# Optimization experiments

Hardware: AMD Instinct MI355X
Metric: run time of the kernel (lower is better)

The kernel has to match this reference:

```python
import jax, jax.numpy as jnp
import numpy as np
from jax import lax

STRIDES = (8, 8, 16, 32, 32)
GRIDS = (40, 36, 24, 16, 12)
MIN_SCORE = 0.1
KEEP_SCORE = 0.1
MASK_THR = 0.5
UPDATE_THR = 0.05
SIGMA = 2.0
TOPN = 500
MAX_MASKS = 100
UP = 4


def points_nms(h):
    # max_pool2d(k=2, s=1, p=1) then crop last row/col == pad (1,0) window 2
    m = lax.reduce_window(h, -jnp.inf, lax.max, (1, 1, 2, 2), (1, 1, 1, 1),
                          ((0, 0), (0, 0), (1, 0), (1, 0)))
    return h * (m == h).astype(h.dtype)


def resize_mat(insz, outsz):
    # bilinear align_corners=True interpolation matrix [outsz, insz]
    if outsz > 1:
        src = jnp.arange(outsz, dtype=jnp.float32) * ((insz - 1) / (outsz - 1))
    else:
        src = jnp.zeros((outsz,), jnp.float32)
    lo = jnp.clip(jnp.floor(src).astype(jnp.int32), 0, insz - 1)
    hi = jnp.minimum(lo + 1, insz - 1)
    w = src - lo.astype(jnp.float32)
    r = jnp.arange(outsz)
    M = jnp.zeros((outsz, insz), jnp.float32)
    return M.at[r, lo].add(1.0 - w).at[r, hi].add(w)


def bilinear(x, oh, ow):  # x: [k,h,w]
    Mh = resize_mat(x.shape[1], oh)
    Mw = resize_mat(x.shape[2], ow)
    return jnp.einsum('Ww,kHw->kHW', Mw, jnp.einsum('Hh,khw->kHw', Mh, x))


def prep(cate_preds, kernel_preds):
    B = cate_preds[0].shape[0]
    cate = [points_nms(jax.nn.sigmoid(c)) for c in cate_preds]
    cate_flat = jnp.concatenate(
        [jnp.transpose(c, (0, 2, 3, 1)).reshape(B, -1, c.shape[1]) for c in cate], axis=1)
    kern_flat = jnp.concatenate(
        [jnp.transpose(k, (0, 2, 3, 1)).reshape(B, -1, k.shape[1]) for k in kernel_preds], axis=1)
    strides_vec = jnp.concatenate(
        [jnp.full((g * g,), float(s), jnp.float32) for g, s in zip(GRIDS, STRIDES)])
    return cate_flat, kern_flat, strides_vec


def decode_soft(mask_feat, cate_flat, kern_flat, strides_vec):
    # fixed-shape (padded) version of the per-image decode; invalid slots carry score 0
    nc = cate_flat.shape[-1]
    flat = cate_flat.reshape(-1)
    vals, idx = lax.top_k(jnp.where(flat > MIN_SCORE, flat, -1.0), TOPN)
    validk = vals > MIN_SCORE
    cell = idx // nc
    label = idx % nc
    # dynamic 1x1 conv == einsum with gathered kernels
    sig = jax.nn.sigmoid(jnp.einsum('kc,chw->khw', kern_flat[cell], mask_feat))
    binm = (sig > MASK_THR).astype(sig.dtype)
    summ = binm.sum((1, 2))
    keep = validk & (summ > strides_vec[cell])
    seg = (sig * binm).sum((1, 2)) / jnp.maximum(summ, 1e-6)
    scores = jnp.where(keep, vals * seg, 0.0)
    order = jnp.argsort(-scores)
    scores = scores[order]
    sig = sig[order]
    label = label[order]
    keep_o = keep[order]
    summ = jnp.where(keep, summ, 0.0)[order]
    binm = binm[order] * keep_o[:, None, None].astype(binm.dtype)
    # matrix NMS (gaussian)
    flatm = binm.reshape(TOPN, -1)
    inter = flatm @ flatm.T
    iou = inter / jnp.maximum(summ[:, None] + summ[None, :] - inter, 1e-6)
    triu = jnp.triu(jnp.ones((TOPN, TOPN), bool), 1)
    dmat = jnp.where(triu & (label[:, None] == label[None, :]), iou, 0.0)
    comp = dmat.max(0)  # max suppression each item received
    coef = (jnp.exp(-SIGMA * dmat**2) / jnp.exp(-SIGMA * comp[:, None]**2)).min(0)
    s2 = scores * coef
    s2 = jnp.where((s2 >= UPDATE_THR) & (s2 >= KEEP_SCORE) & keep_o, s2, 0.0)
    fv, fi = lax.top_k(s2, MAX_MASKS)
    return fv, jnp.where(fv > 0, label[fi], -1), sig[fi]


def reference(mask_feat_pred, cate_pred_0, cate_pred_1, cate_pred_2, cate_pred_3,
              cate_pred_4, kernel_pred_0, kernel_pred_1, kernel_pred_2, kernel_pred_3,
              kernel_pred_4, scaled_sizes, origin_sizes):
    cate_preds = [cate_pred_0, cate_pred_1, cate_pred_2, cate_pred_3, cate_pred_4]
    kernel_preds = [kernel_pred_0, kernel_pred_1, kernel_pred_2, kernel_pred_3, kernel_pred_4]
    cate_flat, kern_flat, sv = prep(cate_preds, kernel_preds)
    fv, lab, sig = jax.vmap(lambda mf, cf, kf: decode_soft(mf, cf, kf, sv))(
        mask_feat_pred, cate_flat, kern_flat)
    H = mask_feat_pred.shape[2] * UP
    W = mask_feat_pred.shape[3] * UP
    up = jax.vmap(lambda s: bilinear(s, H, W))(sig)  # [B,M,H,W]
    sh, sw = int(scaled_sizes[0, 0]), int(scaled_sizes[0, 1])
    oh, ow = int(origin_sizes[0, 0]), int(origin_sizes[0, 1])
    up = up[:, :, :sh, :sw]
    up = jax.vmap(lambda s: bilinear(s, oh, ow))(up)
    masks = ((up > MASK_THR) & (fv > 0)[:, :, None, None]).astype(jnp.uint8)
    return masks, lab, fv


def setup_inputs() -> dict:
    key = jax.random.key(0)
    ks = jax.random.split(key, 11)
    B, C, NC, HM = 2, 256, 80, 128
    inp = {'mask_feat_pred': jax.random.normal(ks[0], (B, C, HM, HM), jnp.float32)}
    for i, g in enumerate(GRIDS):
        inp[f'cate_pred_{i}'] = jax.random.normal(ks[1 + i], (B, NC, g, g), jnp.float32)
        inp[f'kernel_pred_{i}'] = jax.random.normal(ks[6 + i], (B, C, g, g), jnp.float32) * 0.05
    inp['scaled_sizes'] = jnp.full((B, 2), HM * UP, jnp.int32)
    inp['origin_sizes'] = jnp.full((B, 2), HM * UP, jnp.int32)
    return inp
```

## Files before the change

### kernel.cpp

```cpp
#include <hip/hip_runtime.h>
#include <math.h>
#include <stdint.h>

#define NBATCH 2
#define NC 80
#define CHN 256
#define HMM 128
#define HWN (HMM*HMM)
#define NCELL 3872
#define FLATN (NCELL*NC)
#define TOPN 500
#define SROWS 512
#define MAXM 100
#define OUTH 512
#define OUTW 512
#define NBINS 1024
#define CANDCAP 2048
#define BM 128
#define BN2 256
#define BK 32
#define GNB (HWN/BN2)

__device__ __forceinline__ float sigmoidf_(float x){ return 1.0f/(1.0f+expf(-x)); }

__device__ __forceinline__ void cell_decode(int cell, int& lvl, int& g, int& y, int& x){
  int off;
  if (cell < 1600)      { lvl=0; g=40; off=0; }
  else if (cell < 2896) { lvl=1; g=36; off=1600; }
  else if (cell < 3472) { lvl=2; g=24; off=2896; }
  else if (cell < 3728) { lvl=3; g=16; off=3472; }
  else                  { lvl=4; g=12; off=3728; }
  int r = cell - off; y = r / g; x = r - y*g;
}

template<int N, int NT>
__device__ __forceinline__ void bitonic_desc(uint64_t* key){
  int tid = threadIdx.x;
  for (int k = 2; k <= N; k <<= 1)
    for (int j = k >> 1; j > 0; j >>= 1) {
      __syncthreads();
      for (int e = tid; e < N; e += NT) {
        int l = e ^ j;
        if (l > e) {
          uint64_t a = key[e], c = key[l];
          bool up = ((e & k) == 0);
          if (up ? (a < c) : (a > c)) { key[e] = c; key[l] = a; }
        }
      }
    }
  __syncthreads();
}

__global__ void k0_init(uint32_t* hist, uint32_t* cnt){
  int t = blockIdx.x*blockDim.x + threadIdx.x;
  if (t < NBATCH*NBINS) hist[t] = 0;
  if (t < NBATCH) cnt[t] = 0;
}

__global__ void k1_scores(const float* __restrict__ c0, const float* __restrict__ c1,
                          const float* __restrict__ c2, const float* __restrict__ c3,
                          const float* __restrict__ c4,
                          float* __restrict__ scores, uint32_t* __restrict__ hist){
  int t = blockIdx.x*blockDim.x + threadIdx.x;
  if (t >= NBATCH*FLATN) return;
  int b = t / FLATN;
  int rem = t - b*FLATN;
  int cell = rem / NC;
  int c = rem - cell*NC;
  int lvl,g,y,x; cell_decode(cell,lvl,g,y,x);
  const float* cp = lvl==0?c0:lvl==1?c1:lvl==2?c2:lvl==3?c3:c4;
  const float* base = cp + (size_t)(b*NC + c)*g*g;
  float raw = base[y*g + x];
  float m = raw;
  if (y > 0)          m = fmaxf(m, base[(y-1)*g + x]);
  if (x > 0)          m = fmaxf(m, base[y*g + x-1]);
  if (y > 0 && x > 0) m = fmaxf(m, base[(y-1)*g + x-1]);
  float s = (raw == m) ? sigmoidf_(raw) : 0.0f;
  scores[t] = s;
  if (s > 0.1f) {
    int bin = (int)(s * 1024.0f); if (bin > NBINS-1) bin = NBINS-1;
    atomicAdd(&hist[b*NBINS + bin], 1u);
  }
}

__global__ __launch_bounds__(1024) void k2_cutoff(const uint32_t* __restrict__ hist, int* __restrict__ cutoff){
  __shared__ uint32_t h[NBINS];
  int b = blockIdx.x;
  h[threadIdx.x] = hist[b*NBINS + threadIdx.x];
  __syncthreads();
  if (threadIdx.x == 0) {
    int acc = 0; int cut = 0;
    for (int d = NBINS-1; d >= 0; --d) {
      acc += (int)h[d];
      if (acc >= TOPN) { cut = d; break; }
    }
    cutoff[b] = cut;
  }
}

__global__ void k3_gather(const float* __restrict__ scores, const int* __restrict__ cutoff,
                          uint32_t* __restrict__ cnt, float* __restrict__ cval, uint32_t* __restrict__ cidx){
  int t = blockIdx.x*blockDim.x + threadIdx.x;
  if (t >= NBATCH*FLATN) return;
  int b = t / FLATN; int idx = t - b*FLATN;
  float v = scores[t];
  if (v > 0.1f) {
    int bin = (int)(v * 1024.0f); if (bin > NBINS-1) bin = NBINS-1;
    if (bin >= cutoff[b]) {
      uint32_t p = atomicAdd(&cnt[b], 1u);
      if (p < CANDCAP) { cval[b*CANDCAP+p] = v; cidx[b*CANDCAP+p] = (uint32_t)idx; }
    }
  }
}

__global__ __launch_bounds__(1024) void k4_sort(const uint32_t* __restrict__ cnt,
        const float* __restrict__ cval, const uint32_t* __restrict__ cidx,
        float* __restrict__ vals, int* __restrict__ cellA, int* __restrict__ labelA){
  __shared__ uint64_t key[CANDCAP];
  int b = blockIdx.x; int tid = threadIdx.x;
  int n = (int)cnt[b]; if (n > CANDCAP) n = CANDCAP;
  for (int e = tid; e < CANDCAP; e += 1024) {
    uint64_t k = 0;
    if (e < n)
      k = ((uint64_t)__float_as_uint(cval[b*CANDCAP+e]) << 32) |
          (uint64_t)(0xFFFFFFFFu - cidx[b*CANDCAP+e]);
    key[e] = k;
  }
  bitonic_desc<CANDCAP,1024>(key);
  for (int r = tid; r < TOPN; r += 1024) {
    uint64_t k = key[r];
    if ((k >> 32) == 0) { vals[b*TOPN+r] = -1.0f; cellA[b*TOPN+r] = 0; labelA[b*TOPN+r] = 0; }
    else {
      uint32_t idx = 0xFFFFFFFFu - (uint32_t)(k & 0xFFFFFFFFu);
      vals[b*TOPN+r]   = __uint_as_float((uint32_t)(k >> 32));
      cellA[b*TOPN+r]  = (int)(idx / NC);
      labelA[b*TOPN+r] = (int)(idx % NC);
    }
  }
}

__global__ void k5_kmat(const float* __restrict__ k0p, const float* __restrict__ k1p,
                        const float* __restrict__ k2p, const float* __restrict__ k3p,
                        const float* __restrict__ k4p,
                        const int* __restrict__ cellA, float* __restrict__ Kmat){
  int t = blockIdx.x*blockDim.x + threadIdx.x;
  if (t >= NBATCH*TOPN*CHN) return;
  int b = t / (TOPN*CHN); int rem = t - b*(TOPN*CHN);
  int k = rem / CHN; int c = rem - k*CHN;
  int cell = cellA[b*TOPN + k];
  int lvl,g,y,x; cell_decode(cell,lvl,g,y,x);
  const float* kp = lvl==0?k0p:lvl==1?k1p:lvl==2?k2p:lvl==3?k3p:k4p;
  Kmat[t] = kp[((size_t)(b*CHN + c)*g + y)*g + x];
}

__global__ __launch_bounds__(256, 2) void k6_gemm1(const float* __restrict__ Kmat, const float* __restrict__ mf,
        float* __restrict__ sigfull, uint32_t* __restrict__ bits,
        float* __restrict__ psum, float* __restrict__ pseg){
  __shared__ alignas(16) float As[BK][BM+4];
  __shared__ alignas(16) float Bs[BK][BN2];
  __shared__ uint32_t bitsL[BM][8];
  int tid = threadIdx.x;
  int nb = blockIdx.x, mb = blockIdx.y, b = blockIdx.z;
  int row0 = mb*BM, col0 = nb*BN2;
  int tx = tid & 15, ty = tid >> 4;
  for (int i = tid; i < BM*8; i += 256) ((uint32_t*)bitsL)[i] = 0;

  int ar[4], aq[4], bkk[8], bcc[8];
  #pragma unroll
  for (int i = 0; i < 4; ++i) { int e = i*256 + tid; ar[i] = e >> 3; aq[i] = e & 7; }
  #pragma unroll
  for (int i = 0; i < 8; ++i) { int e = i*256 + tid; bkk[i] = e >> 6; bcc[i] = e & 63; }

  float4 pa[4], pb[8];
  const float4 z4 = make_float4(0.f,0.f,0.f,0.f);
  #pragma unroll
  for (int i = 0; i < 4; ++i) {
    int rr = row0 + ar[i];
    pa[i] = (rr < TOPN) ? *(const float4*)&Kmat[((size_t)b*TOPN + rr)*CHN + aq[i]*4] : z4;
  }
  #pragma unroll
  for (int i = 0; i < 8; ++i)
    pb[i] = *(const float4*)&mf[((size_t)b*CHN + bkk[i])*HWN + col0 + bcc[i]*4];

  float acc[8][16];
  #pragma unroll
  for (int i=0;i<8;i++)
    #pragma unroll
    for(int j=0;j<16;j++) acc[i][j]=0.f;

  for (int k0 = 0; k0 < CHN; k0 += BK) {
    __syncthreads();
    #pragma unroll
    for (int i = 0; i < 4; ++i) {
      int colA = ar[i] ^ (aq[i] << 2);
      As[aq[i]*4+0][colA] = pa[i].x;
      As[aq[i]*4+1][colA] = pa[i].y;
      As[aq[i]*4+2][colA] = pa[i].z;
      As[aq[i]*4+3][colA] = pa[i].w;
    }
    #pragma unroll
    for (int i = 0; i < 8; ++i)
      *(float4*)&Bs[bkk[i]][bcc[i]*4] = pb[i];
    __syncthreads();
    if (k0 + BK < CHN) {
      int k0n = k0 + BK;
      #pragma unroll
      for (int i = 0; i < 4; ++i) {
        int rr = row0 + ar[i];
        pa[i] = (rr < TOPN) ? *(const float4*)&Kmat[((size_t)b*TOPN + rr)*CHN + k0n + aq[i]*4] : z4;
      }
      #pragma unroll
      for (int i = 0; i < 8; ++i)
        pb[i] = *(const float4*)&mf[((size_t)b*CHN + k0n + bkk[i])*HWN + col0 + bcc[i]*4];
    }
    #pragma unroll 2
    for (int kk = 0; kk < BK; ++kk) {
      int s = (kk >> 2) << 2;
      float4 a0 = *(float4*)&As[kk][(ty*8) ^ s];
      float4 a1 = *(float4*)&As[kk][(ty*8+4) ^ s];
      float av[8] = {a0.x,a0.y,a0.z,a0.w,a1.x,a1.y,a1.z,a1.w};
      #pragma unroll
      for (int q = 0; q < 4; ++q) {
        float4 bv = *(float4*)&Bs[kk][q*64 + tx*4];
        #pragma unroll
        for (int i = 0; i < 8; ++i) {
          acc[i][q*4+0] += av[i]*bv.x;
          acc[i][q*4+1] += av[i]*bv.y;
          acc[i][q*4+2] += av[i]*bv.z;
          acc[i][q*4+3] += av[i]*bv.w;
        }
      }
    }
  }
  #pragma unroll
  for (int i = 0; i < 8; ++i) {
    int r = row0 + ty*8 + i;
    float se = 0.f; int cc = 0;
    #pragma unroll
    for (int q = 0; q < 4; ++q) {
      float4 sv;
      sv.x = sigmoidf_(acc[i][q*4+0]);
      sv.y = sigmoidf_(acc[i][q*4+1]);
      sv.z = sigmoidf_(acc[i][q*4+2]);
      sv.w = sigmoidf_(acc[i][q*4+3]);
      uint32_t m = 0;
      if (sv.x > 0.5f) { m |= 1u; se += sv.x; cc++; }
      if (sv.y > 0.5f) { m |= 2u; se += sv.y; cc++; }
      if (sv.z > 0.5f) { m |= 4u; se += sv.z; cc++; }
      if (sv.w > 0.5f) { m |= 8u; se += sv.w; cc++; }
      atomicOr(&bitsL[ty*8+i][2*q + (tx>>3)], m << ((tx&7)*4));
      *(float4*)&sigfull[((size_t)b*SROWS + r)*HWN + col0 + q*64 + tx*4] = sv;
    }
    #pragma unroll
    for (int d = 1; d < 16; d <<= 1) {
      se += __shfl_xor(se, d);
      cc += __shfl_xor(cc, d);
    }
    if (tx == 0 && r < TOPN) {
      psum[((size_t)b*TOPN + r)*GNB + nb] = (float)cc;
      pseg[((size_t)b*TOPN + r)*GNB + nb] = se;
    }
  }
  __syncthreads();
  for (int e = tid; e < BM*8; e += 256) {
    int rr = e >> 3, w = e & 7;
    if (row0 + rr < TOPN)
      bits[((size_t)b*TOPN + row0 + rr)*512 + nb*8 + w] = bitsL[rr][w];
  }
}

__global__ void k7_rowstats(const float* __restrict__ psum, const float* __restrict__ pseg,
                            const float* __restrict__ vals, const int* __restrict__ cellA,
                            float* __restrict__ summ, float* __restrict__ scores, int* __restrict__ keepA){
  int t = blockIdx.x*blockDim.x + threadIdx.x;
  if (t >= NBATCH*TOPN) return;
  float sc = 0.f, sg = 0.f;
  for (int i = 0; i < GNB; i += 4) {
    float4 a = *(const float4*)&psum[(size_t)t*GNB+i];
    float4 c = *(const float4*)&pseg[(size_t)t*GNB+i];
    sc += a.x+a.y+a.z+a.w; sg += c.x+c.y+c.z+c.w;
  }
  float v = vals[t];
  int cell = cellA[t];
  int lvl,g,y,x; cell_decode(cell,lvl,g,y,x);
  float stride = (lvl<=1)?8.f:(lvl==2)?16.f:32.f;
  bool keep = (v > 0.1f) && (sc > stride);
  float seg = sg / fmaxf(sc, 1e-6f);
  summ[t] = sc;
  scores[t] = keep ? v*seg : 0.f;
  keepA[t] = keep ? 1 : 0;
}

__global__ __launch_bounds__(512) void k8_order(const float* __restrict__ scores, int* __restrict__ order){
  __shared__ uint64_t key[512];
  int b = blockIdx.x, tid = threadIdx.x;
  uint64_t k = 0;
  if (tid < TOPN)
    k = ((uint64_t)__float_as_uint(scores[b*TOPN+tid]) << 32) | (uint64_t)(0xFFFFFFFFu - (uint32_t)tid);
  key[tid] = k;
  bitonic_desc<512,512>(key);
  if (tid < TOPN) order[b*TOPN+tid] = (int)(0xFFFFFFFFu - (uint32_t)(key[tid] & 0xFFFFFFFFu));
}

__global__ __launch_bounds__(256) void k9_dmat(const uint32_t* __restrict__ bitsG,
        const int* __restrict__ order, const int* __restrict__ labelA, const int* __restrict__ keepA,
        const float* __restrict__ summ, float* __restrict__ dmatT){
  __shared__ uint32_t rowb[512];
  int i = blockIdx.x, b = blockIdx.y, tid = threadIdx.x;
  int oi = order[b*TOPN + i];
  if (!keepA[b*TOPN + oi]) return;
  float si = summ[b*TOPN + oi];
  int li = labelA[b*TOPN + oi];
  for (int w = tid; w < 512; w += 256) rowb[w] = bitsG[((size_t)b*TOPN + oi)*512 + w];
  __syncthreads();
  for (int j = i + 1 + tid; j < TOPN; j += 256) {
    int oj = order[b*TOPN + j];
    if (!keepA[b*TOPN + oj] || labelA[b*TOPN + oj] != li) continue;
    const uint4* rj = (const uint4*)&bitsG[((size_t)b*TOPN + oj)*512];
    const uint4* ri = (const uint4*)rowb;
    int cc = 0;
    for (int w = 0; w < 128; ++w) {
      uint4 x = rj[w], y = ri[w];
      cc += __popc(x.x & y.x) + __popc(x.y & y.y) + __popc(x.z & y.z) + __popc(x.w & y.w);
    }
    float sj = summ[b*TOPN + oj];
    float inter = (float)cc;
    dmatT[((size_t)b*TOPN + j)*TOPN + i] = inter / fmaxf(si + sj - inter, 1e-6f);
  }
}

__global__ __launch_bounds__(256) void k10_comp(const float* __restrict__ dmatT,
        float* __restrict__ comp, float* __restrict__ e2c){
  __shared__ float red[4];
  int j = blockIdx.x, b = blockIdx.y, tid = threadIdx.x;
  float m = 0.f;
  for (int i = tid; i < TOPN; i += 256) m = fmaxf(m, dmatT[((size_t)b*TOPN+j)*TOPN + i]);
  #pragma unroll
  for (int d = 1; d < 64; d <<= 1) m = fmaxf(m, __shfl_xor(m, d));
  if ((tid & 63) == 0) red[tid >> 6] = m;
  __syncthreads();
  if (tid == 0) {
    m = fmaxf(fmaxf(red[0], red[1]), fmaxf(red[2], red[3]));
    comp[b*TOPN+j] = m;
    e2c[b*TOPN+j] = expf(-2.0f*m*m);
  }
}

__global__ __launch_bounds__(256) void k10_coef(const float* __restrict__ dmatT, const float* __restrict__ e2c,
        const float* __restrict__ scores, const int* __restrict__ order, const int* __restrict__ keepA,
        float* __restrict__ s2){
  __shared__ float red[4];
  int j = blockIdx.x, b = blockIdx.y, tid = threadIdx.x;
  float mn = 1e30f;
  for (int i = tid; i < TOPN; i += 256) {
    float d = dmatT[((size_t)b*TOPN+j)*TOPN + i];
    float r = expf(-2.0f*d*d) / e2c[b*TOPN+i];
    mn = fminf(mn, r);
  }
  #pragma unroll
  for (int d = 1; d < 64; d <<= 1) mn = fminf(mn, __shfl_xor(mn, d));
  if ((tid & 63) == 0) red[tid >> 6] = mn;
  __syncthreads();
  if (tid == 0) {
    mn = fminf(fminf(red[0], red[1]), fminf(red[2], red[3]));
    int oj = order[b*TOPN+j];
    float s = scores[b*TOPN+oj] * mn;
    bool ok = (s >= 0.05f) && (s >= 0.1f) && (keepA[b*TOPN+oj] != 0);
    s2[b*TOPN+j] = ok ? s : 0.f;
  }
}

__global__ __launch_bounds__(512) void k11_top100(const float* __restrict__ s2, const int* __restrict__ order,
        const int* __restrict__ labelA, float* __restrict__ outF, int* __restrict__ selrow){
  __shared__ uint64_t key[512];
  int b = blockIdx.x, tid = threadIdx.x;
  uint64_t k = 0;
  if (tid < TOPN)
    k = ((uint64_t)__float_as_uint(s2[b*TOPN+tid]) << 32) | (uint64_t)(0xFFFFFFFFu - (uint32_t)tid);
  key[tid] = k;
  bitonic_desc<512,512>(key);
  if (tid < MAXM) {
    uint64_t kk = key[tid];
    float v = __uint_as_float((uint32_t)(kk >> 32));
    int j = (int)(0xFFFFFFFFu - (uint32_t)(kk & 0xFFFFFFFFu));
    if (j < 0 || j >= TOPN) { j = 0; v = 0.f; }
    int orow = order[b*TOPN + j];
    float lab = (v > 0.f) ? (float)labelA[b*TOPN + orow] : -1.0f;
    size_t maskCount = (size_t)NBATCH*MAXM*OUTH*OUTW;
    outF[maskCount + (size_t)b*MAXM + tid] = lab;
    outF[maskCount + (size_t)NBATCH*MAXM + (size_t)b*MAXM + tid] = v;
    selrow[b*MAXM + tid] = orow;
  }
}

__global__ void k13_upsample(const float* __restrict__ sigfull, const int* __restrict__ selrow,
                             float* __restrict__ outF){
  int t = blockIdx.x*blockDim.x + threadIdx.x;
  const int XG = OUTW/4;
  int total = NBATCH*MAXM*OUTH*XG;
  if (t >= total) return;
  int xg = t % XG;
  int tmp = t / XG;
  int Y = tmp % OUTH;
  int tmp2 = tmp / OUTH;
  int r = tmp2 % MAXM;
  int b = tmp2 / MAXM;
  size_t maskCount = (size_t)NBATCH*MAXM*OUTH*OUTW;
  float fv = outF[maskCount + (size_t)NBATCH*MAXM + (size_t)b*MAXM + r];
  float4 o = make_float4(0.f,0.f,0.f,0.f);
  if (fv > 0.f) {
    const float* sm = sigfull + ((size_t)b*SROWS + selrow[b*MAXM + r])*HWN;
    const float SC = (float)(127.0/511.0);
    float fy = (float)Y * SC;
    int ly = (int)floorf(fy); if (ly < 0) ly = 0; if (ly > HMM-1) ly = HMM-1;
    int hy = ly+1 < HMM ? ly+1 : HMM-1;
    float wy = fy - (float)ly;
    float res[4];
    #pragma unroll
    for (int u = 0; u < 4; ++u) {
      int X = xg*4 + u;
      float fx = (float)X * SC;
      int lx = (int)floorf(fx); if (lx < 0) lx = 0; if (lx > HMM-1) lx = HMM-1;
      int hx = lx+1 < HMM ? lx+1 : HMM-1;
      float wx = fx - (float)lx;
      float a = (1.f-wy)*sm[ly*HMM+lx] + wy*sm[hy*HMM+lx];
      float c = (1.f-wy)*sm[ly*HMM+hx] + wy*sm[hy*HMM+hx];
      float v = (1.f-wx)*a + wx*c;
      res[u] = (v > 0.5f) ? 1.f : 0.f;
    }
    o = make_float4(res[0],res[1],res[2],res[3]);
  }
  *(float4*)&outF[(((size_t)b*MAXM + r)*OUTH + Y)*OUTW + xg*4] = o;
}

extern "C" void kernel_launch(void* const* d_in, const int* in_sizes, int n_in,
                              void* d_out, int out_size, void* d_ws, size_t ws_size,
                              hipStream_t stream) {
  const float* mf = (const float*)d_in[0];
  const float *cate[5], *kern[5];
  bool interleaved = (n_in > 2) && (in_sizes[2] == NBATCH*CHN*40*40);
  if (interleaved) {
    for (int i = 0; i < 5; ++i) { cate[i] = (const float*)d_in[1 + 2*i]; kern[i] = (const float*)d_in[2 + 2*i]; }
  } else {
    for (int i = 0; i < 5; ++i) { cate[i] = (const float*)d_in[1 + i]; kern[i] = (const float*)d_in[6 + i]; }
  }
  float* outF = (float*)d_out;

  uint8_t* p = (uint8_t*)d_ws;
  auto alloc = [&](size_t bytes) -> void* {
    void* r = (void*)p;
    p += (bytes + 255) & ~(size_t)255;
    return r;
  };
  float*    cate_scores = (float*)   alloc((size_t)NBATCH*FLATN*4);
  uint32_t* hist        = (uint32_t*)alloc((size_t)NBATCH*NBINS*4);
  uint32_t* cnt         = (uint32_t*)alloc((size_t)NBATCH*4);
  int*      cutoff      = (int*)     alloc((size_t)NBATCH*4);
  float*    cval        = (float*)   alloc((size_t)NBATCH*CANDCAP*4);
  uint32_t* cidx        = (uint32_t*)alloc((size_t)NBATCH*CANDCAP*4);
  float*    vals        = (float*)   alloc((size_t)NBATCH*TOPN*4);
  int*      cellA       = (int*)     alloc((size_t)NBATCH*TOPN*4);
  int*      labelA      = (int*)     alloc((size_t)NBATCH*TOPN*4);
  float*    Kmat        = (float*)   alloc((size_t)NBATCH*TOPN*CHN*4);
  uint32_t* bits        = (uint32_t*)alloc((size_t)NBATCH*TOPN*512*4);
  float*    psum        = (float*)   alloc((size_t)NBATCH*TOPN*GNB*4);
  float*    pseg        = (float*)   alloc((size_t)NBATCH*TOPN*GNB*4);
  float*    summ        = (float*)   alloc((size_t)NBATCH*TOPN*4);
  float*    scores      = (float*)   alloc((size_t)NBATCH*TOPN*4);
  int*      keepA       = (int*)     alloc((size_t)NBATCH*TOPN*4);
  int*      order       = (int*)     alloc((size_t)NBATCH*TOPN*4);
  float*    dmatT       = (float*)   alloc((size_t)NBATCH*TOPN*TOPN*4);
  float*    comp        = (float*)   alloc((size_t)NBATCH*TOPN*4);
  float*    e2c         = (float*)   alloc((size_t)NBATCH*TOPN*4);
  float*    s2          = (float*)   alloc((size_t)NBATCH*TOPN*4);
  int*      selrow      = (int*)     alloc((size_t)NBATCH*MAXM*4);
  float*    sigfull     = (float*)   alloc((size_t)NBATCH*SROWS*HWN*4);
  (void)ws_size; (void)out_size;

  hipLaunchKernelGGL(k0_init, dim3((NBATCH*NBINS + 255)/256), dim3(256), 0, stream, hist, cnt);
  hipLaunchKernelGGL(k1_scores, dim3((NBATCH*FLATN + 255)/256), dim3(256), 0, stream,
                     cate[0], cate[1], cate[2], cate[3], cate[4], cate_scores, hist);
  hipLaunchKernelGGL(k2_cutoff, dim3(NBATCH), dim3(1024), 0, stream, hist, cutoff);
  hipLaunchKernelGGL(k3_gather, dim3((NBATCH*FLATN + 255)/256), dim3(256), 0, stream,
                     cate_scores, cutoff, cnt, cval, cidx);
  hipLaunchKernelGGL(k4_sort, dim3(NBATCH), dim3(1024), 0, stream, cnt, cval, cidx, vals, cellA, labelA);
  hipLaunchKernelGGL(k5_kmat, dim3((NBATCH*TOPN*CHN + 255)/256), dim3(256), 0, stream,
                     kern[0], kern[1], kern[2], kern[3], kern[4], cellA, Kmat);
  hipLaunchKernelGGL(k6_gemm1, dim3(HWN/BN2, (TOPN+BM-1)/BM, NBATCH), dim3(256), 0, stream,
                     Kmat, mf, sigfull, bits, psum, pseg);
  hipLaunchKernelGGL(k7_rowstats, dim3((NBATCH*TOPN + 255)/256), dim3(256), 0, stream,
                     psum, pseg, vals, cellA, summ, scores, keepA);
  hipLaunchKernelGGL(k8_order, dim3(NBATCH), dim3(512), 0, stream, scores, order);
  hipMemsetAsync(dmatT, 0, (size_t)NBATCH*TOPN*TOPN*4, stream);
  hipLaunchKernelGGL(k9_dmat, dim3(TOPN, NBATCH), dim3(256), 0, stream,
                     bits, order, labelA, keepA, summ, dmatT);
  hipLaunchKernelGGL(k10_comp, dim3(TOPN, NBATCH), dim3(256), 0, stream, dmatT, comp, e2c);
  hipLaunchKernelGGL(k10_coef, dim3(TOPN, NBATCH), dim3(256), 0, stream,
                     dmatT, e2c, scores, order, keepA, s2);
  hipLaunchKernelGGL(k11_top100, dim3(NBATCH), dim3(512), 0, stream, s2, order, labelA, outF, selrow);
  hipLaunchKernelGGL(k13_upsample, dim3((NBATCH*MAXM*OUTH*(OUTW/4) + 255)/256), dim3(256), 0, stream,
                     sigfull, selrow, outF);
}
```

Measured before the change: 390.3 us.

## Fuse rowstats with ordering, register-prefetch LDS in GEMM, replace atomics with shuffles

Several unrelated changes. The init kernel becomes a memset. The GEMM inner loop double-buffers its LDS reads in registers and is unrolled further. The shared-memory atomicOr bit packing becomes warp shuffles plus a single store. The rowstats and sort kernels are fused into one launch, and the dmat memset is dropped because the dmat kernel now writes zeros to every entry itself. The aims are fewer launches and less LDS latency and contention, at the cost of more GEMM register pressure and full-matrix writes from k9.

```diff
diff --git a/kernel.cpp b/kernel.cpp
--- a/kernel.cpp
+++ b/kernel.cpp
@@ -49,12 +49,6 @@
       }
     }
   __syncthreads();
-}
-
-__global__ void k0_init(uint32_t* hist, uint32_t* cnt){
-  int t = blockIdx.x*blockDim.x + threadIdx.x;
-  if (t < NBATCH*NBINS) hist[t] = 0;
-  if (t < NBATCH) cnt[t] = 0;
 }
 
 __global__ void k1_scores(const float* __restrict__ c0, const float* __restrict__ c1,
@@ -163,7 +157,6 @@
   int nb = blockIdx.x, mb = blockIdx.y, b = blockIdx.z;
   int row0 = mb*BM, col0 = nb*BN2;
   int tx = tid & 15, ty = tid >> 4;
-  for (int i = tid; i < BM*8; i += 256) ((uint32_t*)bitsL)[i] = 0;
 
   int ar[4], aq[4], bkk[8], bcc[8];
   #pragma unroll
@@ -187,6 +180,15 @@
   for (int i=0;i<8;i++)
     #pragma unroll
     for(int j=0;j<16;j++) acc[i][j]=0.f;
+
+  #define LDSRD(KK, A0, A1, B0, B1, B2, B3) { \
+    int s_ = ((KK) >> 2) << 2; \
+    A0 = *(float4*)&As[KK][(ty*8) ^ s_]; \
+    A1 = *(float4*)&As[KK][(ty*8+4) ^ s_]; \
+    B0 = *(float4*)&Bs[KK][tx*4]; \
+    B1 = *(float4*)&Bs[KK][64 + tx*4]; \
+    B2 = *(float4*)&Bs[KK][128 + tx*4]; \
+    B3 = *(float4*)&Bs[KK][192 + tx*4]; }
 
   for (int k0 = 0; k0 < CHN; k0 += BK) {
     __syncthreads();
@@ -213,23 +215,20 @@
       for (int i = 0; i < 8; ++i)
         pb[i] = *(const float4*)&mf[((size_t)b*CHN + k0n + bkk[i])*HWN + col0 + bcc[i]*4];
     }
-    #pragma unroll 2
+    float4 ca0,ca1,cb0,cb1,cb2,cb3, na0,na1,nb0,nb1,nb2,nb3;
+    LDSRD(0, ca0,ca1,cb0,cb1,cb2,cb3);
+    #pragma unroll 8
     for (int kk = 0; kk < BK; ++kk) {
-      int s = (kk >> 2) << 2;
-      float4 a0 = *(float4*)&As[kk][(ty*8) ^ s];
-      float4 a1 = *(float4*)&As[kk][(ty*8+4) ^ s];
-      float av[8] = {a0.x,a0.y,a0.z,a0.w,a1.x,a1.y,a1.z,a1.w};
+      if (kk + 1 < BK) LDSRD(kk+1, na0,na1,nb0,nb1,nb2,nb3);
+      float av[8] = {ca0.x,ca0.y,ca0.z,ca0.w,ca1.x,ca1.y,ca1.z,ca1.w};
       #pragma unroll
-      for (int q = 0; q < 4; ++q) {
-        float4 bv = *(float4*)&Bs[kk][q*64 + tx*4];
-        #pragma unroll
-        for (int i = 0; i < 8; ++i) {
-          acc[i][q*4+0] += av[i]*bv.x;
-          acc[i][q*4+1] += av[i]*bv.y;
-          acc[i][q*4+2] += av[i]*bv.z;
-          acc[i][q*4+3] += av[i]*bv.w;
-        }
+      for (int i = 0; i < 8; ++i) {
+        acc[i][0]  += av[i]*cb0.x; acc[i][1]  += av[i]*cb0.y; acc[i][2]  += av[i]*cb0.z; acc[i][3]  += av[i]*cb0.w;
+        acc[i][4]  += av[i]*cb1.x; acc[i][5]  += av[i]*cb1.y; acc[i][6]  += av[i]*cb1.z; acc[i][7]  += av[i]*cb1.w;
+        acc[i][8]  += av[i]*cb2.x; acc[i][9]  += av[i]*cb2.y; acc[i][10] += av[i]*cb2.z; acc[i][11] += av[i]*cb2.w;
+        acc[i][12] += av[i]*cb3.x; acc[i][13] += av[i]*cb3.y; acc[i][14] += av[i]*cb3.z; acc[i][15] += av[i]*cb3.w;
       }
+      ca0=na0; ca1=na1; cb0=nb0; cb1=nb1; cb2=nb2; cb3=nb3;
     }
   }
   #pragma unroll
@@ -248,7 +247,11 @@
       if (sv.y > 0.5f) { m |= 2u; se += sv.y; cc++; }
       if (sv.z > 0.5f) { m |= 4u; se += sv.z; cc++; }
       if (sv.w > 0.5f) { m |= 8u; se += sv.w; cc++; }
-      atomicOr(&bitsL[ty*8+i][2*q + (tx>>3)], m << ((tx&7)*4));
+      uint32_t wrd = m << ((tx & 7)*4);
+      wrd |= __shfl_xor(wrd, 1);
+      wrd |= __shfl_xor(wrd, 2);
+      wrd |= __shfl_xor(wrd, 4);
+      if ((tx & 7) == 0) bitsL[ty*8+i][2*q + (tx>>3)] = wrd;
       *(float4*)&sigfull[((size_t)b*SROWS + r)*HWN + col0 + q*64 + tx*4] = sv;
     }
     #pragma unroll
@@ -269,34 +272,33 @@
   }
 }
 
-__global__ void k7_rowstats(const float* __restrict__ psum, const float* __restrict__ pseg,
-                            const float* __restrict__ vals, const int* __restrict__ cellA,
-                            float* __restrict__ summ, float* __restrict__ scores, int* __restrict__ keepA){
-  int t = blockIdx.x*blockDim.x + threadIdx.x;
-  if (t >= NBATCH*TOPN) return;
-  float sc = 0.f, sg = 0.f;
-  for (int i = 0; i < GNB; i += 4) {
-    float4 a = *(const float4*)&psum[(size_t)t*GNB+i];
-    float4 c = *(const float4*)&pseg[(size_t)t*GNB+i];
-    sc += a.x+a.y+a.z+a.w; sg += c.x+c.y+c.z+c.w;
-  }
-  float v = vals[t];
-  int cell = cellA[t];
-  int lvl,g,y,x; cell_decode(cell,lvl,g,y,x);
-  float stride = (lvl<=1)?8.f:(lvl==2)?16.f:32.f;
-  bool keep = (v > 0.1f) && (sc > stride);
-  float seg = sg / fmaxf(sc, 1e-6f);
-  summ[t] = sc;
-  scores[t] = keep ? v*seg : 0.f;
-  keepA[t] = keep ? 1 : 0;
-}
-
-__global__ __launch_bounds__(512) void k8_order(const float* __restrict__ scores, int* __restrict__ order){
+__global__ __launch_bounds__(512) void k78_stats_order(const float* __restrict__ psum, const float* __restrict__ pseg,
+        const float* __restrict__ vals, const int* __restrict__ cellA,
+        float* __restrict__ summ, float* __restrict__ scores, int* __restrict__ keepA,
+        int* __restrict__ order){
   __shared__ uint64_t key[512];
   int b = blockIdx.x, tid = threadIdx.x;
   uint64_t k = 0;
-  if (tid < TOPN)
-    k = ((uint64_t)__float_as_uint(scores[b*TOPN+tid]) << 32) | (uint64_t)(0xFFFFFFFFu - (uint32_t)tid);
+  if (tid < TOPN) {
+    int t = b*TOPN + tid;
+    float sc = 0.f, sg = 0.f;
+    for (int i = 0; i < GNB; i += 4) {
+      float4 a = *(const float4*)&psum[(size_t)t*GNB+i];
+      float4 c = *(const float4*)&pseg[(size_t)t*GNB+i];
+      sc += a.x+a.y+a.z+a.w; sg += c.x+c.y+c.z+c.w;
+    }
+    float v = vals[t];
+    int cell = cellA[t];
+    int lvl,g,y,x; cell_decode(cell,lvl,g,y,x);
+    float stride = (lvl<=1)?8.f:(lvl==2)?16.f:32.f;
+    bool keep = (v > 0.1f) && (sc > stride);
+    float seg = sg / fmaxf(sc, 1e-6f);
+    summ[t] = sc;
+    float s = keep ? v*seg : 0.f;
+    scores[t] = s;
+    keepA[t] = keep ? 1 : 0;
+    k = ((uint64_t)__float_as_uint(s) << 32) | (uint64_t)(0xFFFFFFFFu - (uint32_t)tid);
+  }
   key[tid] = k;
   bitonic_desc<512,512>(key);
   if (tid < TOPN) order[b*TOPN+tid] = (int)(0xFFFFFFFFu - (uint32_t)(key[tid] & 0xFFFFFFFFu));
@@ -308,24 +310,29 @@
   __shared__ uint32_t rowb[512];
   int i = blockIdx.x, b = blockIdx.y, tid = threadIdx.x;
   int oi = order[b*TOPN + i];
-  if (!keepA[b*TOPN + oi]) return;
+  int keep_i = keepA[b*TOPN + oi];
   float si = summ[b*TOPN + oi];
   int li = labelA[b*TOPN + oi];
   for (int w = tid; w < 512; w += 256) rowb[w] = bitsG[((size_t)b*TOPN + oi)*512 + w];
   __syncthreads();
-  for (int j = i + 1 + tid; j < TOPN; j += 256) {
-    int oj = order[b*TOPN + j];
-    if (!keepA[b*TOPN + oj] || labelA[b*TOPN + oj] != li) continue;
-    const uint4* rj = (const uint4*)&bitsG[((size_t)b*TOPN + oj)*512];
-    const uint4* ri = (const uint4*)rowb;
-    int cc = 0;
-    for (int w = 0; w < 128; ++w) {
-      uint4 x = rj[w], y = ri[w];
-      cc += __popc(x.x & y.x) + __popc(x.y & y.y) + __popc(x.z & y.z) + __popc(x.w & y.w);
-    }
-    float sj = summ[b*TOPN + oj];
-    float inter = (float)cc;
-    dmatT[((size_t)b*TOPN + j)*TOPN + i] = inter / fmaxf(si + sj - inter, 1e-6f);
+  for (int j = tid; j < TOPN; j += 256) {
+    float v = 0.f;
+    if (keep_i && j > i) {
+      int oj = order[b*TOPN + j];
+      if (keepA[b*TOPN + oj] && labelA[b*TOPN + oj] == li) {
+        const uint4* rj = (const uint4*)&bitsG[((size_t)b*TOPN + oj)*512];
+        const uint4* ri = (const uint4*)rowb;
+        int cc = 0;
+        for (int w = 0; w < 128; ++w) {
+          uint4 x = rj[w], y = ri[w];
+          cc += __popc(x.x & y.x) + __popc(x.y & y.y) + __popc(x.z & y.z) + __popc(x.w & y.w);
+        }
+        float sj = summ[b*TOPN + oj];
+        float inter = (float)cc;
+        v = inter / fmaxf(si + sj - inter, 1e-6f);
+      }
+    }
+    dmatT[((size_t)b*TOPN + j)*TOPN + i] = v;
   }
 }
 
@@ -453,8 +460,8 @@
     return r;
   };
   float*    cate_scores = (float*)   alloc((size_t)NBATCH*FLATN*4);
-  uint32_t* hist        = (uint32_t*)alloc((size_t)NBATCH*NBINS*4);
-  uint32_t* cnt         = (uint32_t*)alloc((size_t)NBATCH*4);
+  uint32_t* hist        = (uint32_t*)alloc((size_t)(NBATCH*NBINS + NBATCH)*4);
+  uint32_t* cnt         = hist + NBATCH*NBINS;
   int*      cutoff      = (int*)     alloc((size_t)NBATCH*4);
   float*    cval        = (float*)   alloc((size_t)NBATCH*CANDCAP*4);
   uint32_t* cidx        = (uint32_t*)alloc((size_t)NBATCH*CANDCAP*4);
@@ -477,7 +484,7 @@
   float*    sigfull     = (float*)   alloc((size_t)NBATCH*SROWS*HWN*4);
   (void)ws_size; (void)out_size;
 
-  hipLaunchKernelGGL(k0_init, dim3((NBATCH*NBINS + 255)/256), dim3(256), 0, stream, hist, cnt);
+  hipMemsetAsync(hist, 0, (size_t)(NBATCH*NBINS + NBATCH)*4, stream);
   hipLaunchKernelGGL(k1_scores, dim3((NBATCH*FLATN + 255)/256), dim3(256), 0, stream,
                      cate[0], cate[1], cate[2], cate[3], cate[4], cate_scores, hist);
   hipLaunchKernelGGL(k2_cutoff, dim3(NBATCH), dim3(1024), 0, stream, hist, cutoff);
@@ -488,10 +495,8 @@
                      kern[0], kern[1], kern[2], kern[3], kern[4], cellA, Kmat);
   hipLaunchKernelGGL(k6_gemm1, dim3(HWN/BN2, (TOPN+BM-1)/BM, NBATCH), dim3(256), 0, stream,
                      Kmat, mf, sigfull, bits, psum, pseg);
-  hipLaunchKernelGGL(k7_rowstats, dim3((NBATCH*TOPN + 255)/256), dim3(256), 0, stream,
-                     psum, pseg, vals, cellA, summ, scores, keepA);
-  hipLaunchKernelGGL(k8_order, dim3(NBATCH), dim3(512), 0, stream, scores, order);
-  hipMemsetAsync(dmatT, 0, (size_t)NBATCH*TOPN*TOPN*4, stream);
+  hipLaunchKernelGGL(k78_stats_order, dim3(NBATCH), dim3(512), 0, stream,
+                     psum, pseg, vals, cellA, summ, scores, keepA, order);
   hipLaunchKernelGGL(k9_dmat, dim3(TOPN, NBATCH), dim3(256), 0, stream,
                      bits, order, labelA, keepA, summ, dmatT);
   hipLaunchKernelGGL(k10_comp, dim3(TOPN, NBATCH), dim3(256), 0, stream, dmatT, comp, e2c);
```

Result: slower. 1.506 ms (+285.9%).
